# Performance work log

Hardware: AMD Instinct MI355X
Metric: run time of the kernel (lower is better)

## Reference

```python
import jax, jax.numpy as jnp
import numpy as np

B, NF, S, L, H, MID, KS, NC, DENSE = 16, 8, 16, 256, 128, 32, 8, 10, 512
COEFF = 0.1
BN_EPS = 1e-5


def _normalize(x):
    return x / jnp.maximum(jnp.linalg.norm(x, axis=-1, keepdims=True), 1e-12)


def _sparsemax(z):
    # sparsemax over last axis (Martins & Astudillo 2016)
    zs = jnp.flip(jnp.sort(z, axis=-1), axis=-1)
    k = jnp.arange(1, z.shape[-1] + 1, dtype=z.dtype)
    cum = jnp.cumsum(zs, axis=-1)
    support = (1.0 + k * zs) > cum
    ksup = jnp.sum(support, axis=-1, keepdims=True)
    tau = (jnp.take_along_axis(cum, ksup - 1, axis=-1) - 1.0) / ksup.astype(z.dtype)
    return jnp.maximum(z - tau, 0.0)


def _bn_ncl(x, g, b, m, v):  # eval-mode BatchNorm1d on [N, C, L]
    return g[None, :, None] * (x - m[None, :, None]) * jax.lax.rsqrt(v[None, :, None] + BN_EPS) + b[None, :, None]


def _bn_nc(x, g, b, m, v):  # eval-mode BatchNorm1d on [N, C]
    return g * (x - m) * jax.lax.rsqrt(v + BN_EPS) + b


def _conv(x, w, pad):
    return jax.lax.conv_general_dilated(x, w, (1,), [(pad, pad)], dimension_numbers=('NCH', 'OIH', 'NCH'))


def _maxpool2(x):  # MaxPool1d(kernel=2, stride=2, padding=1): -inf padded
    return jax.lax.reduce_window(x, -jnp.inf, jax.lax.max, (1, 1, 2), (1, 1, 2), ((0, 0), (0, 0), (1, 1)))


def _cnn(x, cw1, bn1, cw2, bn2, cw3, bn3):
    x = _maxpool2(jax.nn.relu(_bn_ncl(_conv(x, cw1, KS // 2), *bn1)))
    x = _maxpool2(jax.nn.relu(_bn_ncl(_conv(x, cw2, 4), *bn2)))
    x = _maxpool2(jax.nn.relu(_bn_ncl(_conv(x, cw3, 4), *bn3)))
    return jnp.mean(x, axis=-1)  # AdaptiveAvgPool1d(1) -> [N, H]


def _alpha_beta(x, cw1, bn1, cw2, bn2, cw3, bn3, Wq, bq, Wk, bk, Wv, bv):
    b = x.shape[0]
    xf = jnp.transpose(x, (1, 0, 2, 3)).reshape(NF, b * S, 1, L)
    rep = jax.vmap(_cnn)(xf, cw1, bn1, cw2, bn2, cw3, bn3)  # [F, B*S, H]
    rep = rep.reshape(NF, b, S, H)
    Q = jax.nn.elu(rep @ Wq + bq)
    K = jax.nn.leaky_relu(rep @ Wk + bk)
    V = jax.nn.leaky_relu(rep @ Wv + bv)
    # mean_t(Q @ K^T) == Q @ mean_t(K); then scale by sqrt(d_k)
    scores = jnp.einsum('fbsh,fbh->fbs', Q, jnp.mean(K, axis=2)) / jnp.sqrt(jnp.float32(H))
    intra_aw = _sparsemax(scores)                             # [F, B, S]
    Z = _normalize(jnp.einsum('fbs,fbsh->fbh', intra_aw, V))  # [F, B, H]
    Kn = _normalize(rep)
    inter_scores = jnp.einsum('ibh,fbsh->ifbs', Z, Kn)        # cosine scores (Z already unit-norm)
    inter_aw = _sparsemax(inter_scores)                       # [I, F, B, S]
    U = jnp.einsum('ifbs,fbsh->ibh', inter_aw, rep) / NF      # mean over feature axis f
    Hc = _normalize(jnp.concatenate([Z, U], axis=-1))         # [F, B, 2H]
    feat = jnp.transpose(Hc, (1, 0, 2)).reshape(b, NF * 2 * H)
    return feat, intra_aw, inter_aw


def _forward(src_x, src_y, tgt_x, cw1, bn1_g, bn1_b, bn1_m, bn1_v, cw2, bn2_g, bn2_b, bn2_m, bn2_v, cw3, bn3_g, bn3_b, bn3_m, bn3_v, Wq, bq, Wk, bk, Wv, bv, bnc1_g, bnc1_b, bnc1_m, bnc1_v, W1, b1, bnc2_g, bnc2_b, bnc2_m, bnc2_v, W2, b2):
    bn1 = (bn1_g, bn1_b, bn1_m, bn1_v)
    bn2 = (bn2_g, bn2_b, bn2_m, bn2_v)
    bn3 = (bn3_g, bn3_b, bn3_m, bn3_v)
    sf, sa, sb = _alpha_beta(src_x, cw1, bn1, cw2, bn2, cw3, bn3, Wq, bq, Wk, bk, Wv, bv)
    _, ta, tb = _alpha_beta(tgt_x, cw1, bn1, cw2, bn2, cw3, bn3, Wq, bq, Wk, bk, Wv, bv)
    h = _bn_nc(sf, bnc1_g, bnc1_b, bnc1_m, bnc1_v) @ W1 + b1
    h = jax.nn.leaky_relu(_bn_nc(h, bnc2_g, bnc2_b, bnc2_m, bnc2_v))
    y_pred = jax.nn.softmax(h @ W2 + b2, axis=-1)
    # MMD domain losses (detached in original via torch.tensor(list))
    da = jnp.mean(sa - ta, axis=-2)                           # [F, S]
    loss_a = COEFF * jnp.mean(jnp.linalg.norm(da, axis=-1))
    db = jnp.mean(sb - tb, axis=-2)                           # [I, F, S]
    loss_b = COEFF * jnp.mean(jnp.sqrt(jnp.sum(db * db, axis=(1, 2))))
    dom = jax.lax.stop_gradient(loss_a + loss_b)
    # CrossEntropyLoss applied to already-softmaxed preds, as in source
    logp = jax.nn.log_softmax(y_pred, axis=-1)
    ce = -jnp.mean(logp[jnp.arange(y_pred.shape[0]), src_y])
    return y_pred, ce + dom


def setup_inputs() -> dict:
    ks = jax.random.split(jax.random.key(0), 40)
    rn = lambda i, sh, s=1.0: s * jax.random.normal(ks[i], sh, dtype=jnp.float32)
    ru = lambda i, sh, lo, hi: jax.random.uniform(ks[i], sh, jnp.float32, lo, hi)
    return {
        'src_x': rn(0, (B, NF, S, L)),
        'src_y': jax.random.randint(ks[1], (B,), 0, NC),
        'tgt_x': rn(2, (B, NF, S, L)),
        'cw1': rn(3, (NF, MID, 1, KS), 0.1),
        'bn1_g': ru(4, (NF, MID), 0.75, 1.25), 'bn1_b': rn(5, (NF, MID), 0.1),
        'bn1_m': rn(6, (NF, MID), 0.1), 'bn1_v': ru(7, (NF, MID), 0.5, 1.5),
        'cw2': rn(8, (NF, 2 * MID, MID, 8), 0.05),
        'bn2_g': ru(9, (NF, 2 * MID), 0.75, 1.25), 'bn2_b': rn(10, (NF, 2 * MID), 0.1),
        'bn2_m': rn(11, (NF, 2 * MID), 0.1), 'bn2_v': ru(12, (NF, 2 * MID), 0.5, 1.5),
        'cw3': rn(13, (NF, H, 2 * MID, 8), 0.05),
        'bn3_g': ru(14, (NF, H), 0.75, 1.25), 'bn3_b': rn(15, (NF, H), 0.1),
        'bn3_m': rn(16, (NF, H), 0.1), 'bn3_v': ru(17, (NF, H), 0.5, 1.5),
        'Wq': rn(18, (H, H), 0.05), 'bq': rn(19, (H,), 0.02),
        'Wk': rn(20, (H, H), 0.05), 'bk': rn(21, (H,), 0.02),
        'Wv': rn(22, (H, H), 0.05), 'bv': rn(23, (H,), 0.02),
        'bnc1_g': ru(24, (NF * 2 * H,), 0.75, 1.25), 'bnc1_b': rn(25, (NF * 2 * H,), 0.1),
        'bnc1_m': rn(26, (NF * 2 * H,), 0.1), 'bnc1_v': ru(27, (NF * 2 * H,), 0.5, 1.5),
        'W1': rn(28, (NF * 2 * H, DENSE), 0.03), 'b1': rn(29, (DENSE,), 0.02),
        'bnc2_g': ru(30, (DENSE,), 0.75, 1.25), 'bnc2_b': rn(31, (DENSE,), 0.1),
        'bnc2_m': rn(32, (DENSE,), 0.1), 'bnc2_v': ru(33, (DENSE,), 0.5, 1.5),
        'W2': rn(34, (DENSE, NC), 0.05), 'b2': rn(35, (NC,), 0.02),
    }


def reference(src_x, src_y, tgt_x, cw1, bn1_g, bn1_b, bn1_m, bn1_v, cw2, bn2_g, bn2_b, bn2_m, bn2_v, cw3, bn3_g, bn3_b, bn3_m, bn3_v, Wq, bq, Wk, bk, Wv, bv, bnc1_g, bnc1_b, bnc1_m, bnc1_v, W1, b1, bnc2_g, bnc2_b, bnc2_m, bnc2_v, W2, b2):
    return _forward(src_x, src_y, tgt_x, cw1, bn1_g, bn1_b, bn1_m, bn1_v, cw2, bn2_g, bn2_b, bn2_m, bn2_v, cw3, bn3_g, bn3_b, bn3_m, bn3_v, Wq, bq, Wk, bk, Wv, bv, bnc1_g, bnc1_b, bnc1_m, bnc1_v, W1, b1, bnc2_g, bnc2_b, bnc2_m, bnc2_v, W2, b2)
```

## Files before the change

### kernel.cpp

```cpp
#include <hip/hip_runtime.h>

typedef unsigned short u16;
typedef unsigned int u32;
typedef __attribute__((ext_vector_type(8))) short bfrag;
typedef __attribute__((ext_vector_type(4))) float ffrag;

__device__ __forceinline__ float lrelu(float x) { return x >= 0.f ? x : 0.01f * x; }
__device__ __forceinline__ float eluf(float x)  { return x > 0.f ? x : expm1f(x); }
__device__ __forceinline__ u16 f2bf(float f) {
    u32 x = __float_as_uint(f);
    return (u16)((x + 0x7fffu + ((x >> 16) & 1u)) >> 16);
}
__device__ __forceinline__ u16 f2bt(float f) {
    return (u16)(__float_as_uint(f) >> 16);
}
__device__ __forceinline__ float bf2f(u16 u) {
    return __uint_as_float(((u32)u) << 16);
}

__device__ void sparsemax16(const float* z, float* out) {
    float zs[16];
    for (int i = 0; i < 16; ++i) zs[i] = z[i];
    for (int i = 1; i < 16; ++i) {
        float key = zs[i]; int j = i - 1;
        while (j >= 0 && zs[j] < key) { zs[j + 1] = zs[j]; --j; }
        zs[j + 1] = key;
    }
    float cum[16];
    cum[0] = zs[0];
    for (int i = 1; i < 16; ++i) cum[i] = cum[i - 1] + zs[i];
    int ksup = 0;
    for (int k = 1; k <= 16; ++k)
        if (1.0f + (float)k * zs[k - 1] > cum[k - 1]) ksup++;
    if (ksup < 1) ksup = 1;
    float tau = (cum[ksup - 1] - 1.0f) / (float)ksup;
    for (int i = 0; i < 16; ++i) out[i] = fmaxf(z[i] - tau, 0.0f);
}

__global__ __launch_bounds__(256) void k_wprep(
    const float* __restrict__ w2, const float* __restrict__ w3,
    const float* __restrict__ Wq, const float* __restrict__ Wk,
    const float* __restrict__ Wv,
    u16* __restrict__ wpk2, u16* __restrict__ wpk3, u16* __restrict__ wqkv)
{
    int i0 = (blockIdx.x * 256 + threadIdx.x) * 4;
    for (int t = 0; t < 4; ++t) {
        int i = i0 + t;
        if (i < 131072) {
            int j = i & 7, L = (i >> 3) & 63, kc = (i >> 9) & 7, nt = (i >> 12) & 3, f = i >> 14;
            int co = nt * 16 + (L & 15);
            int ci = ((L >> 4) << 3) + j;
            wpk2[i] = f2bf(w2[(((size_t)f * 64 + co) * 32 + ci) * 8 + kc]);
        } else if (i < 131072 + 524288) {
            int i2 = i - 131072;
            int j = i2 & 7, L = (i2 >> 3) & 63, kc = (i2 >> 9) & 15, nt = (i2 >> 13) & 7, f = i2 >> 16;
            int co = nt * 16 + (L & 15);
            int ci = ((kc & 1) << 5) + ((L >> 4) << 3) + j;
            wpk3[i2] = f2bf(w3[(((size_t)f * 128 + co) * 64 + ci) * 8 + (kc >> 1)]);
        } else if (i < 131072 + 524288 + 49152) {
            int j2 = i - 655360;
            int proj = j2 >> 14, idx = j2 & 16383;
            int jj = idx & 7, L = (idx >> 3) & 63, kc = (idx >> 9) & 3, nt = idx >> 11;
            int n = nt * 16 + (L & 15);
            int k = kc * 32 + ((L >> 4) << 3) + jj;
            const float* W = proj == 0 ? Wq : (proj == 1 ? Wk : Wv);
            wqkv[j2] = f2bf(W[k * 128 + n]);
        }
    }
}

#define S1T_STRIDE 40
#define S2T_STRIDE 72
#define RB2_STRIDE 68
#define RB3_STRIDE 140
#define RB_OFF 6336
#define SMEM_U16 (RB_OFF + 67 * RB3_STRIDE)

__global__ __launch_bounds__(256) void k_cnn(
    const float* __restrict__ xs, const float* __restrict__ xt,
    const float* __restrict__ w1, const float* __restrict__ g1, const float* __restrict__ b1,
    const float* __restrict__ m1, const float* __restrict__ v1,
    const float* __restrict__ g2, const float* __restrict__ b2,
    const float* __restrict__ m2, const float* __restrict__ v2,
    const float* __restrict__ g3, const float* __restrict__ b3,
    const float* __restrict__ m3, const float* __restrict__ v3,
    const u16* __restrict__ wpk2, const u16* __restrict__ wpk3,
    float* __restrict__ rep)
{
    __shared__ __align__(16) u16 smem[SMEM_U16];
    float* xin = (float*)(smem + RB_OFF);

    int tid = threadIdx.x, blk = blockIdx.x;
    int pass = blk >> 11, f = (blk >> 8) & 7, n = blk & 255;
    int bb = n >> 4, ss = n & 15;
    int lane = tid & 63, w = tid >> 6;
    const float* x = pass ? xt : xs;
    float* rep_p = rep + (size_t)pass * 262144;

    bfrag B2[8];
    {
        const bfrag* gB = reinterpret_cast<const bfrag*>(wpk2);
        for (int kc = 0; kc < 8; ++kc)
            B2[kc] = gB[(((size_t)f * 4 + w) * 8 + kc) * 64 + lane];
    }

    {
        u32* z = (u32*)smem;
        for (int i = tid; i < 80; i += 256) z[i] = 0;
        for (int i = tid; i < 360; i += 256) z[2660 + i] = 0;
        if (tid < 4) { xin[tid] = 0.f; xin[260 + tid] = 0.f; }
        const float* xr = x + (((size_t)bb * 8 + f) * 16 + ss) * 256;
        for (int i = tid; i < 256; i += 256) xin[i + 4] = xr[i];
    }
    __syncthreads();

    if (tid < 208) {
        int cc = tid & 7, jc = tid >> 3;
        int co0 = cc * 4, j0 = jc * 5;
        float wr[4][8];
        for (int c = 0; c < 4; ++c) {
            const float4* q = reinterpret_cast<const float4*>(w1 + ((size_t)f * 32 + co0 + c) * 8);
            float4 a = q[0], bq = q[1];
            wr[c][0] = a.x; wr[c][1] = a.y; wr[c][2] = a.z; wr[c][3] = a.w;
            wr[c][4] = bq.x; wr[c][5] = bq.y; wr[c][6] = bq.z; wr[c][7] = bq.w;
        }
        int px[10];
        for (int i = 0; i < 10; ++i) {
            int p = 2 * j0 - 1 + i;
            px[i] = p < 0 ? 0 : (p > 256 ? 256 : p);
        }
        float acc[4][10];
        for (int c = 0; c < 4; ++c) for (int i = 0; i < 10; ++i) acc[c][i] = 0.f;
        for (int k = 0; k < 8; ++k) {
            float xv[10];
            for (int i = 0; i < 10; ++i) xv[i] = xin[px[i] + k];
            for (int c = 0; c < 4; ++c)
                for (int i = 0; i < 10; ++i) acc[c][i] += wr[c][k] * xv[i];
        }
        for (int c = 0; c < 4; ++c) {
            int co = co0 + c;
            float sc = g1[f * 32 + co] * rsqrtf(v1[f * 32 + co] + 1e-5f);
            float sh = b1[f * 32 + co] - m1[f * 32 + co] * sc;
            for (int jj = 0; jj < 5; ++jj) {
                int j = j0 + jj;
                if (j < 129) {
                    float a0 = fmaxf(acc[c][2 * jj] * sc + sh, 0.f);
                    float a1 = fmaxf(acc[c][2 * jj + 1] * sc + sh, 0.f);
                    smem[(j + 4) * S1T_STRIDE + co] = f2bt(fmaxf(a0, a1));
                }
            }
        }
    }
    __syncthreads();

    {
        int nt = w;
        int co = nt * 16 + (lane & 15);
        float sc = g2[f * 64 + co] * rsqrtf(v2[f * 64 + co] + 1e-5f);
        float sh = b2[f * 64 + co] - m2[f * 64 + co] * sc;
        int arow = lane & 15, ci0 = (lane >> 4) << 3;
        for (int mt = 0; mt < 9; ++mt) {
            ffrag C = {0.f, 0.f, 0.f, 0.f};
            int rb = mt * 16 + arow;
            for (int kc = 0; kc < 8; ++kc) {
                bfrag A = *reinterpret_cast<const bfrag*>(&smem[(rb + kc) * S1T_STRIDE + ci0]);
                C = __builtin_amdgcn_mfma_f32_16x16x32_bf16(A, B2[kc], C, 0, 0, 0);
            }
            int p0 = mt * 16 + ((lane >> 4) << 2);
            for (int r = 0; r < 4; ++r) {
                int p = p0 + r;
                if (p < 130)
                    smem[RB_OFF + p * RB2_STRIDE + co] = f2bt(fmaxf(C[r] * sc + sh, 0.f));
            }
        }
    }
    __syncthreads();

    {
        u32* z = (u32*)smem;
        for (int i = tid; i < 144; i += 256) z[i] = 0;
        for (int i = tid; i < 612; i += 256) z[2520 + i] = 0;
    }
    for (int e = tid; e < 66 * 64; e += 256) {
        int j = e >> 6, ci = e & 63;
        float vmax;
        if (j == 0) {
            vmax = bf2f(smem[RB_OFF + 0 * RB2_STRIDE + ci]);
        } else if (j == 65) {
            vmax = bf2f(smem[RB_OFF + 129 * RB2_STRIDE + ci]);
        } else {
            float a0 = bf2f(smem[RB_OFF + (2 * j - 1) * RB2_STRIDE + ci]);
            float a1 = bf2f(smem[RB_OFF + (2 * j) * RB2_STRIDE + ci]);
            vmax = fmaxf(a0, a1);
        }
        smem[(j + 4) * S2T_STRIDE + ci] = f2bt(vmax);
    }
    __syncthreads();

    for (int t = 0; t < 2; ++t) {
        int nt = w * 2 + t;
        bfrag B3[16];
        const bfrag* gB = reinterpret_cast<const bfrag*>(wpk3);
        for (int kc = 0; kc < 16; ++kc)
            B3[kc] = gB[(((size_t)f * 8 + nt) * 16 + kc) * 64 + lane];
        int co = nt * 16 + (lane & 15);
        float sc = g3[f * 128 + co] * rsqrtf(v3[f * 128 + co] + 1e-5f);
        float sh = b3[f * 128 + co] - m3[f * 128 + co] * sc;
        int arow = lane & 15, q8 = (lane >> 4) << 3;
        for (int mt = 0; mt < 5; ++mt) {
            ffrag C = {0.f, 0.f, 0.f, 0.f};
            int rb = mt * 16 + arow;
            for (int kc = 0; kc < 16; ++kc) {
                int row = rb + (kc >> 1);
                int ci0 = ((kc & 1) << 5) + q8;
                bfrag A = *reinterpret_cast<const bfrag*>(&smem[row * S2T_STRIDE + ci0]);
                C = __builtin_amdgcn_mfma_f32_16x16x32_bf16(A, B3[kc], C, 0, 0, 0);
            }
            int p0 = mt * 16 + ((lane >> 4) << 2);
            for (int r = 0; r < 4; ++r) {
                int p = p0 + r;
                if (p < 67)
                    smem[RB_OFF + p * RB3_STRIDE + co] = f2bt(fmaxf(C[r] * sc + sh, 0.f));
            }
        }
    }
    __syncthreads();

    if (tid < 128) {
        int co = tid;
        float sum = bf2f(smem[RB_OFF + 0 * RB3_STRIDE + co]);
        for (int j = 1; j < 34; ++j) {
            float a0 = bf2f(smem[RB_OFF + (2 * j - 1) * RB3_STRIDE + co]);
            float a1 = bf2f(smem[RB_OFF + (2 * j) * RB3_STRIDE + co]);
            sum += fmaxf(a0, a1);
        }
        rep_p[(((size_t)f * 256) + n) * 128 + co] = sum * (1.0f / 34.0f);
    }
}

__global__ __launch_bounds__(256) void k_attn1(
    const float* __restrict__ rep, const u16* __restrict__ wqkv,
    const float* __restrict__ bq, const float* __restrict__ bk,
    const float* __restrict__ bv,
    float* __restrict__ Zn, float* __restrict__ rninv, float* __restrict__ iaw)
{
    __shared__ __align__(16) u16 repbf[16 * 136];
    __shared__ float KmL[128], ZL[128], awL[16], scoresL[16], r2L[16];
    __shared__ float spart[4][4][4];
    __shared__ float redL[4];
    int tid = threadIdx.x;
    int pass = blockIdx.x >> 7, f = (blockIdx.x >> 4) & 7, b = blockIdx.x & 15;
    const float* rp = rep + (size_t)pass * 262144 + ((size_t)f * 256 + b * 16) * 128;
    float* Zn_p = Zn + (size_t)pass * 16384;
    float* rninv_p = rninv + (size_t)pass * 2048;
    float* iaw_p = iaw + (size_t)pass * 2048;

    {
        int s = tid >> 4, i = tid & 15, h0 = i * 8;
        const float4* q4 = reinterpret_cast<const float4*>(rp + s * 128 + h0);
        float4 a = q4[0], c = q4[1];
        float p2 = a.x*a.x + a.y*a.y + a.z*a.z + a.w*a.w
                 + c.x*c.x + c.y*c.y + c.z*c.z + c.w*c.w;
        bfrag pk;
        pk[0] = (short)f2bt(a.x); pk[1] = (short)f2bt(a.y);
        pk[2] = (short)f2bt(a.z); pk[3] = (short)f2bt(a.w);
        pk[4] = (short)f2bt(c.x); pk[5] = (short)f2bt(c.y);
        pk[6] = (short)f2bt(c.z); pk[7] = (short)f2bt(c.w);
        *reinterpret_cast<bfrag*>(&repbf[s * 136 + h0]) = pk;
        p2 += __shfl_xor(p2, 1); p2 += __shfl_xor(p2, 2);
        p2 += __shfl_xor(p2, 4); p2 += __shfl_xor(p2, 8);
        if (i == 0) r2L[s] = p2;
    }
    __syncthreads();

    int lane = tid & 63, w = tid >> 6, arow = lane & 15, q = lane >> 4;
    bfrag A[4];
    for (int kc = 0; kc < 4; ++kc)
        A[kc] = *reinterpret_cast<const bfrag*>(&repbf[arow * 136 + kc * 32 + q * 8]);

    float qv[2][4], vvv[2][4];
    int colv[2];
    const bfrag* BB = reinterpret_cast<const bfrag*>(wqkv);
    for (int t = 0; t < 2; ++t) {
        int nt = w * 2 + t;
        ffrag cq = {0.f,0.f,0.f,0.f}, ck = {0.f,0.f,0.f,0.f}, cv = {0.f,0.f,0.f,0.f};
        for (int kc = 0; kc < 4; ++kc) {
            int fi = (nt * 4 + kc) * 64 + lane;
            bfrag Bq = BB[fi];
            bfrag Bk = BB[2048 + fi];
            bfrag Bv = BB[4096 + fi];
            cq = __builtin_amdgcn_mfma_f32_16x16x32_bf16(A[kc], Bq, cq, 0, 0, 0);
            ck = __builtin_amdgcn_mfma_f32_16x16x32_bf16(A[kc], Bk, ck, 0, 0, 0);
            cv = __builtin_amdgcn_mfma_f32_16x16x32_bf16(A[kc], Bv, cv, 0, 0, 0);
        }
        int col = nt * 16 + arow;
        colv[t] = col;
        float bqc = bq[col], bkc = bk[col], bvc = bv[col];
        float kpt = 0.f;
        for (int r = 0; r < 4; ++r) {
            qv[t][r] = eluf(cq[r] + bqc);
            vvv[t][r] = lrelu(cv[r] + bvc);
            kpt += lrelu(ck[r] + bkc);
        }
        kpt += __shfl_xor(kpt, 16);
        kpt += __shfl_xor(kpt, 32);
        if (q == 0) KmL[col] = kpt * (1.f / 16.f);
    }
    __syncthreads();

    {
        float km0 = KmL[colv[0]], km1 = KmL[colv[1]];
        float ps[4];
        for (int r = 0; r < 4; ++r) {
            float v = qv[0][r] * km0 + qv[1][r] * km1;
            v += __shfl_xor(v, 1); v += __shfl_xor(v, 2);
            v += __shfl_xor(v, 4); v += __shfl_xor(v, 8);
            ps[r] = v;
        }
        if (arow == 0)
            for (int r = 0; r < 4; ++r) spart[w][q][r] = ps[r];
    }
    __syncthreads();
    if (tid < 16) {
        int qq = tid >> 2, rr = tid & 3;
        float sc = spart[0][qq][rr] + spart[1][qq][rr] + spart[2][qq][rr] + spart[3][qq][rr];
        scoresL[tid] = sc * 0.08838834764831845f;
        rninv_p[f * 256 + b * 16 + tid] = 1.f / fmaxf(sqrtf(r2L[tid]), 1e-12f);
    }
    __syncthreads();
    if (tid == 0) sparsemax16(scoresL, awL);
    __syncthreads();
    if (tid < 16) iaw_p[f * 256 + b * 16 + tid] = awL[tid];

    for (int t = 0; t < 2; ++t) {
        float zp = 0.f;
        for (int r = 0; r < 4; ++r) zp += awL[q * 4 + r] * vvv[t][r];
        zp += __shfl_xor(zp, 16);
        zp += __shfl_xor(zp, 32);
        if (q == 0) ZL[colv[t]] = zp;
    }
    __syncthreads();
    if (tid < 128) {
        float z = ZL[tid];
        float v = z * z;
        v += __shfl_xor(v, 1); v += __shfl_xor(v, 2); v += __shfl_xor(v, 4);
        v += __shfl_xor(v, 8); v += __shfl_xor(v, 16); v += __shfl_xor(v, 32);
        if (lane == 0) redL[w] = v;
    }
    __syncthreads();
    if (tid == 0) redL[2] = 1.f / fmaxf(sqrtf(redL[0] + redL[1]), 1e-12f);
    __syncthreads();
    if (tid < 128)
        Zn_p[((size_t)f * 16 + b) * 128 + tid] = ZL[tid] * redL[2];
}

__global__ __launch_bounds__(256) void k_attn2(
    const float* __restrict__ rep, const float* __restrict__ Zn,
    const float* __restrict__ rninv, float* __restrict__ ibw,
    const float* __restrict__ g, const float* __restrict__ bb,
    const float* __restrict__ mm, const float* __restrict__ vv,
    float* __restrict__ featbn)
{
    __shared__ float repL[16384];
    __shared__ float ZiL[128], scores[128], UL[128];
    __shared__ float awLf[8][16];
    __shared__ float redL[2];
    int tid = threadIdx.x, blk = blockIdx.x;
    int pass = blk >> 7, b = (blk >> 3) & 15, i = blk & 7;
    const float* rep_p = rep + (size_t)pass * 262144;

    for (int f = 0; f < 8; ++f) {
        const float4* src = reinterpret_cast<const float4*>(
            rep_p + ((size_t)f * 256 + b * 16) * 128);
        float4* dst = reinterpret_cast<float4*>(repL + f * 2048);
        for (int t = tid; t < 512; t += 256) dst[t] = src[t];
    }
    if (tid < 128) ZiL[tid] = Zn[(size_t)pass * 16384 + ((size_t)i * 16 + b) * 128 + tid];
    __syncthreads();

    if (tid < 128) {
        int f = tid >> 4, s = tid & 15;
        const float* rr = repL + tid * 128;
        float a = 0.f;
        for (int h = 0; h < 128; ++h) a += ZiL[h] * rr[h];
        scores[tid] = a * rninv[(size_t)pass * 2048 + f * 256 + b * 16 + s];
    }
    __syncthreads();
    if (tid < 8) {
        float aw[16];
        sparsemax16(&scores[tid * 16], aw);
        for (int s = 0; s < 16; ++s) awLf[tid][s] = aw[s];
    }
    __syncthreads();
    if (tid < 128) {
        int f = tid >> 4, s = tid & 15;
        ibw[(size_t)pass * 16384 + (((size_t)i * 8 + f) * 16 + b) * 16 + s] = awLf[f][s];
    }
    if (pass == 0) {
        if (tid < 128) {
            int h = tid;
            float u = 0.f;
            for (int f = 0; f < 8; ++f) {
                const float* rr = repL + f * 2048 + h;
                const float* aa = awLf[f];
                for (int s = 0; s < 16; ++s) u += aa[s] * rr[s * 128];
            }
            UL[h] = u * 0.125f;
        }
        __syncthreads();
        if (tid < 128) {
            int lane = tid & 63, w = tid >> 6;
            float v = ZiL[tid] * ZiL[tid] + UL[tid] * UL[tid];
            v += __shfl_xor(v, 1); v += __shfl_xor(v, 2); v += __shfl_xor(v, 4);
            v += __shfl_xor(v, 8); v += __shfl_xor(v, 16); v += __shfl_xor(v, 32);
            if (lane == 0) redL[w] = v;
        }
        __syncthreads();
        if (tid < 256) {
            float inv = 1.f / fmaxf(sqrtf(redL[0] + redL[1]), 1e-12f);
            int d = tid;
            int e = i * 256 + d;
            float val = (d < 128 ? ZiL[d] : UL[d - 128]) * inv;
            float scv = g[e] * rsqrtf(vv[e] + 1e-5f);
            featbn[b * 2048 + e] = (val - mm[e]) * scv + bb[e];
        }
    }
}

__global__ __launch_bounds__(256) void k_head1(
    const float* __restrict__ featbn,
    const float* __restrict__ W1, const float* __restrict__ b1,
    const float* __restrict__ g2, const float* __restrict__ bb2,
    const float* __restrict__ mm2, const float* __restrict__ vv2,
    float* __restrict__ h2ws)
{
    __shared__ float featL[2048];
    __shared__ float part[32][32];
    int tid = threadIdx.x, blk = blockIdx.x;
    int b = blk >> 4, cc = blk & 15;
    {
        const float4* src = reinterpret_cast<const float4*>(featbn + b * 2048);
        float4* dst = reinterpret_cast<float4*>(featL);
        for (int i = tid; i < 512; i += 256) dst[i] = src[i];
    }
    __syncthreads();
    int ks = tid >> 3, cg = tid & 7;
    int col0 = cc * 32 + cg * 4;
    float4 acc = {0.f, 0.f, 0.f, 0.f};
    const float* fl = featL + ks * 64;
    for (int c = 0; c < 64; ++c) {
        int k = ks * 64 + c;
        float4 wv = *reinterpret_cast<const float4*>(W1 + (size_t)k * 512 + col0);
        float fv = fl[c];
        acc.x += fv * wv.x; acc.y += fv * wv.y;
        acc.z += fv * wv.z; acc.w += fv * wv.w;
    }
    part[ks][cg * 4 + 0] = acc.x;
    part[ks][cg * 4 + 1] = acc.y;
    part[ks][cg * 4 + 2] = acc.z;
    part[ks][cg * 4 + 3] = acc.w;
    __syncthreads();
    if (tid < 32) {
        int colw = cc * 32 + tid;
        float s = b1[colw];
        for (int k2 = 0; k2 < 32; ++k2) s += part[k2][tid];
        float scv = g2[colw] * rsqrtf(vv2[colw] + 1e-5f);
        float val = (s - mm2[colw]) * scv + bb2[colw];
        h2ws[b * 512 + colw] = lrelu(val);
    }
}

__global__ __launch_bounds__(256) void k_tail(
    const float* __restrict__ h2ws,
    const float* __restrict__ W2, const float* __restrict__ b2,
    const float* __restrict__ sa, const float* __restrict__ ta,
    const float* __restrict__ sb, const float* __restrict__ tb,
    const int* __restrict__ sy, float* __restrict__ dout)
{
    __shared__ float h2L[8192];
    __shared__ float lgL[160], ypL[160];
    __shared__ float sA[8], sB[8];
    int tid = threadIdx.x;
    for (int i = tid; i < 8192; i += 256) h2L[i] = h2ws[i];
    if (tid < 8) { sA[tid] = 0.f; sB[tid] = 0.f; }
    __syncthreads();
    if (tid < 160) {
        int b = tid / 10, j = tid - b * 10;
        float a = b2[j];
        const float* h = h2L + b * 512;
        for (int c = 0; c < 512; ++c) a += h[c] * W2[c * 10 + j];
        lgL[tid] = a;
    }
    __syncthreads();
    if (tid < 16) {
        int b = tid;
        float mx = lgL[b * 10];
        for (int j = 1; j < 10; ++j) mx = fmaxf(mx, lgL[b * 10 + j]);
        float sum = 0.f, ex[10];
        for (int j = 0; j < 10; ++j) { ex[j] = expf(lgL[b * 10 + j] - mx); sum += ex[j]; }
        for (int j = 0; j < 10; ++j) {
            float p = ex[j] / sum;
            ypL[b * 10 + j] = p;
            dout[b * 10 + j] = p;
        }
    }
    __syncthreads();
    if (tid < 128) {
        int f = tid >> 4, s = tid & 15;
        float d = 0.f;
        for (int b = 0; b < 16; ++b) d += sa[f * 256 + b * 16 + s] - ta[f * 256 + b * 16 + s];
        d *= (1.f / 16.f);
        atomicAdd(&sA[f], d * d);
    }
    for (int e = tid; e < 1024; e += 256) {
        int i = e >> 7, f = (e >> 4) & 7, s = e & 15;
        float d = 0.f;
        int base = ((i * 8 + f) * 16) * 16 + s;
        for (int b = 0; b < 16; ++b) d += sb[base + b * 16] - tb[base + b * 16];
        d *= (1.f / 16.f);
        atomicAdd(&sB[i], d * d);
    }
    __syncthreads();
    if (tid == 0) {
        float la = 0.f, lb = 0.f;
        for (int f = 0; f < 8; ++f) la += sqrtf(sA[f]);
        for (int i = 0; i < 8; ++i) lb += sqrtf(sB[i]);
        la *= 0.1f / 8.f;
        lb *= 0.1f / 8.f;
        float ce = 0.f;
        for (int b = 0; b < 16; ++b) {
            const float* y = ypL + b * 10;
            float mx = y[0];
            for (int j = 1; j < 10; ++j) mx = fmaxf(mx, y[j]);
            float sum = 0.f;
            for (int j = 0; j < 10; ++j) sum += expf(y[j] - mx);
            float lse = mx + logf(sum);
            ce += lse - y[sy[b]];
        }
        ce *= (1.f / 16.f);
        dout[160] = ce + la + lb;
    }
}

extern "C" void kernel_launch(void* const* d_in, const int* in_sizes, int n_in,
                              void* d_out, int out_size, void* d_ws, size_t ws_size,
                              hipStream_t stream) {
    (void)in_sizes; (void)n_in; (void)out_size; (void)ws_size;
    const float* src_x = (const float*)d_in[0];
    const int*   src_y = (const int*)d_in[1];
    const float* tgt_x = (const float*)d_in[2];
    const float *cw1 = (const float*)d_in[3], *bn1g = (const float*)d_in[4],
                *bn1b = (const float*)d_in[5], *bn1m = (const float*)d_in[6],
                *bn1v = (const float*)d_in[7];
    const float *cw2 = (const float*)d_in[8], *bn2g = (const float*)d_in[9],
                *bn2b = (const float*)d_in[10], *bn2m = (const float*)d_in[11],
                *bn2v = (const float*)d_in[12];
    const float *cw3 = (const float*)d_in[13], *bn3g = (const float*)d_in[14],
                *bn3b = (const float*)d_in[15], *bn3m = (const float*)d_in[16],
                *bn3v = (const float*)d_in[17];
    const float *Wq = (const float*)d_in[18], *bq = (const float*)d_in[19],
                *Wk = (const float*)d_in[20], *bk = (const float*)d_in[21],
                *Wv = (const float*)d_in[22], *bv = (const float*)d_in[23];
    const float *bc1g = (const float*)d_in[24], *bc1b = (const float*)d_in[25],
                *bc1m = (const float*)d_in[26], *bc1v = (const float*)d_in[27];
    const float *W1 = (const float*)d_in[28], *b1 = (const float*)d_in[29];
    const float *bc2g = (const float*)d_in[30], *bc2b = (const float*)d_in[31],
                *bc2m = (const float*)d_in[32], *bc2v = (const float*)d_in[33];
    const float *W2 = (const float*)d_in[34], *b2 = (const float*)d_in[35];

    float* ws = (float*)d_ws;
    size_t o = 0;
    float* rep    = ws + o; o += (size_t)2 * 262144;
    float* Zn     = ws + o; o += (size_t)2 * 16384;
    float* rninv  = ws + o; o += (size_t)2 * 2048;
    float* ia     = ws + o; o += (size_t)2 * 2048;
    float* ib     = ws + o; o += (size_t)2 * 16384;
    float* featbn = ws + o; o += (size_t)16 * 2048;
    float* h2ws   = ws + o; o += (size_t)16 * 512;
    u16* wpk2 = (u16*)(ws + o); o += 65536;
    u16* wpk3 = (u16*)(ws + o); o += 262144;
    u16* wqkv = (u16*)(ws + o); o += 24576;

    k_wprep<<<688, 256, 0, stream>>>(cw2, cw3, Wq, Wk, Wv, wpk2, wpk3, wqkv);
    k_cnn<<<4096, 256, 0, stream>>>(src_x, tgt_x,
        cw1, bn1g, bn1b, bn1m, bn1v,
        bn2g, bn2b, bn2m, bn2v,
        bn3g, bn3b, bn3m, bn3v,
        wpk2, wpk3, rep);
    k_attn1<<<256, 256, 0, stream>>>(rep, wqkv, bq, bk, bv, Zn, rninv, ia);
    k_attn2<<<256, 256, 0, stream>>>(rep, Zn, rninv, ib, bc1g, bc1b, bc1m, bc1v, featbn);
    k_head1<<<256, 256, 0, stream>>>(featbn, W1, b1, bc2g, bc2b, bc2m, bc2v, h2ws);
    k_tail<<<1, 256, 0, stream>>>(h2ws, W2, b2, ia, ia + 2048, ib, ib + 16384,
                                  src_y, (float*)d_out);
}
```

Before: 311.8 us.

## Fuse intra and inter attention kernels into a single launch

Merges k_attn1 and k_attn2 into one kernel. Each block loads the full 8-feature rep tile into shared memory, computes row norms there, and runs the intra-attention for feature i of batch b, then the inter-attention. Zn and rninv no longer go through global memory, and one launch plus its dependency gap is removed. The cost is redundant norm computation across blocks and a larger shared-memory footprint in the QKV phase.

```diff
diff --git a/kernel.cpp b/kernel.cpp
--- a/kernel.cpp
+++ b/kernel.cpp
@@ -238,42 +238,53 @@
     }
 }
 
-__global__ __launch_bounds__(256) void k_attn1(
+__global__ __launch_bounds__(256) void k_attn(
     const float* __restrict__ rep, const u16* __restrict__ wqkv,
     const float* __restrict__ bq, const float* __restrict__ bk,
     const float* __restrict__ bv,
-    float* __restrict__ Zn, float* __restrict__ rninv, float* __restrict__ iaw)
+    float* __restrict__ iaw, float* __restrict__ ibw,
+    const float* __restrict__ g, const float* __restrict__ bb,
+    const float* __restrict__ mm, const float* __restrict__ vv,
+    float* __restrict__ featbn)
 {
+    __shared__ float repL[16384];
     __shared__ __align__(16) u16 repbf[16 * 136];
-    __shared__ float KmL[128], ZL[128], awL[16], scoresL[16], r2L[16];
+    __shared__ float rinvL[128], KmL[128], ZnL[128];
+    __shared__ float awL[16], scoresL[16];
     __shared__ float spart[4][4][4];
     __shared__ float redL[4];
-    int tid = threadIdx.x;
-    int pass = blockIdx.x >> 7, f = (blockIdx.x >> 4) & 7, b = blockIdx.x & 15;
-    const float* rp = rep + (size_t)pass * 262144 + ((size_t)f * 256 + b * 16) * 128;
-    float* Zn_p = Zn + (size_t)pass * 16384;
-    float* rninv_p = rninv + (size_t)pass * 2048;
+    __shared__ float scores2[128], UL[128], awLf[8][16], redB[2];
+
+    int tid = threadIdx.x, blk = blockIdx.x;
+    int pass = blk >> 7, b = (blk >> 3) & 15, i = blk & 7;
+    int lane = tid & 63, w = tid >> 6, arow = lane & 15, q = lane >> 4;
+    const float* rep_p = rep + (size_t)pass * 262144;
     float* iaw_p = iaw + (size_t)pass * 2048;
-
-    {
-        int s = tid >> 4, i = tid & 15, h0 = i * 8;
-        const float4* q4 = reinterpret_cast<const float4*>(rp + s * 128 + h0);
-        float4 a = q4[0], c = q4[1];
-        float p2 = a.x*a.x + a.y*a.y + a.z*a.z + a.w*a.w
-                 + c.x*c.x + c.y*c.y + c.z*c.z + c.w*c.w;
+    float* ibw_p = ibw + (size_t)pass * 16384;
+
+    for (int f = 0; f < 8; ++f) {
+        const float4* src = reinterpret_cast<const float4*>(
+            rep_p + ((size_t)f * 256 + b * 16) * 128);
+        float4* dst = reinterpret_cast<float4*>(repL + f * 2048);
+        for (int t = tid; t < 512; t += 256) dst[t] = src[t];
+    }
+    __syncthreads();
+
+    if (tid < 128) {
+        const float* r = repL + tid * 128;
+        float s = 0.f;
+        for (int h = 0; h < 128; ++h) { float v = r[h]; s += v * v; }
+        rinvL[tid] = 1.f / fmaxf(sqrtf(s), 1e-12f);
+    }
+    {
+        int s = tid >> 4, ii = tid & 15, h0 = ii * 8;
+        const float* r = repL + (i * 16 + s) * 128 + h0;
         bfrag pk;
-        pk[0] = (short)f2bt(a.x); pk[1] = (short)f2bt(a.y);
-        pk[2] = (short)f2bt(a.z); pk[3] = (short)f2bt(a.w);
-        pk[4] = (short)f2bt(c.x); pk[5] = (short)f2bt(c.y);
-        pk[6] = (short)f2bt(c.z); pk[7] = (short)f2bt(c.w);
+        for (int j = 0; j < 8; ++j) pk[j] = (short)f2bt(r[j]);
         *reinterpret_cast<bfrag*>(&repbf[s * 136 + h0]) = pk;
-        p2 += __shfl_xor(p2, 1); p2 += __shfl_xor(p2, 2);
-        p2 += __shfl_xor(p2, 4); p2 += __shfl_xor(p2, 8);
-        if (i == 0) r2L[s] = p2;
-    }
-    __syncthreads();
-
-    int lane = tid & 63, w = tid >> 6, arow = lane & 15, q = lane >> 4;
+    }
+    __syncthreads();
+
     bfrag A[4];
     for (int kc = 0; kc < 4; ++kc)
         A[kc] = *reinterpret_cast<const bfrag*>(&repbf[arow * 136 + kc * 32 + q * 8]);
@@ -325,23 +336,22 @@
         int qq = tid >> 2, rr = tid & 3;
         float sc = spart[0][qq][rr] + spart[1][qq][rr] + spart[2][qq][rr] + spart[3][qq][rr];
         scoresL[tid] = sc * 0.08838834764831845f;
-        rninv_p[f * 256 + b * 16 + tid] = 1.f / fmaxf(sqrtf(r2L[tid]), 1e-12f);
     }
     __syncthreads();
     if (tid == 0) sparsemax16(scoresL, awL);
     __syncthreads();
-    if (tid < 16) iaw_p[f * 256 + b * 16 + tid] = awL[tid];
+    if (tid < 16) iaw_p[i * 256 + b * 16 + tid] = awL[tid];
 
     for (int t = 0; t < 2; ++t) {
         float zp = 0.f;
         for (int r = 0; r < 4; ++r) zp += awL[q * 4 + r] * vvv[t][r];
         zp += __shfl_xor(zp, 16);
         zp += __shfl_xor(zp, 32);
-        if (q == 0) ZL[colv[t]] = zp;
+        if (q == 0) ZnL[colv[t]] = zp;
     }
     __syncthreads();
     if (tid < 128) {
-        float z = ZL[tid];
+        float z = ZnL[tid];
         float v = z * z;
         v += __shfl_xor(v, 1); v += __shfl_xor(v, 2); v += __shfl_xor(v, 4);
         v += __shfl_xor(v, 8); v += __shfl_xor(v, 16); v += __shfl_xor(v, 32);
@@ -350,51 +360,25 @@
     __syncthreads();
     if (tid == 0) redL[2] = 1.f / fmaxf(sqrtf(redL[0] + redL[1]), 1e-12f);
     __syncthreads();
-    if (tid < 128)
-        Zn_p[((size_t)f * 16 + b) * 128 + tid] = ZL[tid] * redL[2];
-}
-
-__global__ __launch_bounds__(256) void k_attn2(
-    const float* __restrict__ rep, const float* __restrict__ Zn,
-    const float* __restrict__ rninv, float* __restrict__ ibw,
-    const float* __restrict__ g, const float* __restrict__ bb,
-    const float* __restrict__ mm, const float* __restrict__ vv,
-    float* __restrict__ featbn)
-{
-    __shared__ float repL[16384];
-    __shared__ float ZiL[128], scores[128], UL[128];
-    __shared__ float awLf[8][16];
-    __shared__ float redL[2];
-    int tid = threadIdx.x, blk = blockIdx.x;
-    int pass = blk >> 7, b = (blk >> 3) & 15, i = blk & 7;
-    const float* rep_p = rep + (size_t)pass * 262144;
-
-    for (int f = 0; f < 8; ++f) {
-        const float4* src = reinterpret_cast<const float4*>(
-            rep_p + ((size_t)f * 256 + b * 16) * 128);
-        float4* dst = reinterpret_cast<float4*>(repL + f * 2048);
-        for (int t = tid; t < 512; t += 256) dst[t] = src[t];
-    }
-    if (tid < 128) ZiL[tid] = Zn[(size_t)pass * 16384 + ((size_t)i * 16 + b) * 128 + tid];
-    __syncthreads();
-
+    if (tid < 128) ZnL[tid] = ZnL[tid] * redL[2];
+    __syncthreads();
+
+    if (tid < 128) {
+        const float* rr = repL + tid * 128;
+        float a = 0.f;
+        for (int h = 0; h < 128; ++h) a += ZnL[h] * rr[h];
+        scores2[tid] = a * rinvL[tid];
+    }
+    __syncthreads();
+    if (tid < 8) {
+        float aw[16];
+        sparsemax16(&scores2[tid * 16], aw);
+        for (int s = 0; s < 16; ++s) awLf[tid][s] = aw[s];
+    }
+    __syncthreads();
     if (tid < 128) {
         int f = tid >> 4, s = tid & 15;
-        const float* rr = repL + tid * 128;
-        float a = 0.f;
-        for (int h = 0; h < 128; ++h) a += ZiL[h] * rr[h];
-        scores[tid] = a * rninv[(size_t)pass * 2048 + f * 256 + b * 16 + s];
-    }
-    __syncthreads();
-    if (tid < 8) {
-        float aw[16];
-        sparsemax16(&scores[tid * 16], aw);
-        for (int s = 0; s < 16; ++s) awLf[tid][s] = aw[s];
-    }
-    __syncthreads();
-    if (tid < 128) {
-        int f = tid >> 4, s = tid & 15;
-        ibw[(size_t)pass * 16384 + (((size_t)i * 8 + f) * 16 + b) * 16 + s] = awLf[f][s];
+        ibw_p[(((size_t)i * 8 + f) * 16 + b) * 16 + s] = awLf[f][s];
     }
     if (pass == 0) {
         if (tid < 128) {
@@ -409,18 +393,17 @@
         }
         __syncthreads();
         if (tid < 128) {
-            int lane = tid & 63, w = tid >> 6;
-            float v = ZiL[tid] * ZiL[tid] + UL[tid] * UL[tid];
+            float v = ZnL[tid] * ZnL[tid] + UL[tid] * UL[tid];
             v += __shfl_xor(v, 1); v += __shfl_xor(v, 2); v += __shfl_xor(v, 4);
             v += __shfl_xor(v, 8); v += __shfl_xor(v, 16); v += __shfl_xor(v, 32);
-            if (lane == 0) redL[w] = v;
+            if (lane == 0) redB[w] = v;
         }
         __syncthreads();
-        if (tid < 256) {
-            float inv = 1.f / fmaxf(sqrtf(redL[0] + redL[1]), 1e-12f);
+        {
+            float inv = 1.f / fmaxf(sqrtf(redB[0] + redB[1]), 1e-12f);
             int d = tid;
             int e = i * 256 + d;
-            float val = (d < 128 ? ZiL[d] : UL[d - 128]) * inv;
+            float val = (d < 128 ? ZnL[d] : UL[d - 128]) * inv;
             float scv = g[e] * rsqrtf(vv[e] + 1e-5f);
             featbn[b * 2048 + e] = (val - mm[e]) * scv + bb[e];
         }
@@ -571,8 +554,6 @@
     float* ws = (float*)d_ws;
     size_t o = 0;
     float* rep    = ws + o; o += (size_t)2 * 262144;
-    float* Zn     = ws + o; o += (size_t)2 * 16384;
-    float* rninv  = ws + o; o += (size_t)2 * 2048;
     float* ia     = ws + o; o += (size_t)2 * 2048;
     float* ib     = ws + o; o += (size_t)2 * 16384;
     float* featbn = ws + o; o += (size_t)16 * 2048;
@@ -587,8 +568,8 @@
         bn2g, bn2b, bn2m, bn2v,
         bn3g, bn3b, bn3m, bn3v,
         wpk2, wpk3, rep);
-    k_attn1<<<256, 256, 0, stream>>>(rep, wqkv, bq, bk, bv, Zn, rninv, ia);
-    k_attn2<<<256, 256, 0, stream>>>(rep, Zn, rninv, ib, bc1g, bc1b, bc1m, bc1v, featbn);
+    k_attn<<<256, 256, 0, stream>>>(rep, wqkv, bq, bk, bv, ia, ib,
+                                    bc1g, bc1b, bc1m, bc1v, featbn);
     k_head1<<<256, 256, 0, stream>>>(featbn, W1, b1, bc2g, bc2b, bc2m, bc2v, h2ws);
     k_tail<<<1, 256, 0, stream>>>(h2ws, W2, b2, ia, ia + 2048, ib, ib + 16384,
                                   src_y, (float*)d_out);
```

New measurement: 316.8 us. No clear change (+1.6%).
